# Optimization experiments

Measured on AMD Instinct MI355X. Metric: run time of the kernel, lower is better.

## Reference

```python
import jax, jax.numpy as jnp
import numpy as np

N, F_IN, F_OUT = 8192, 256, 256
ALPHA = 0.2  # LeakyReLU negative slope
NEG = -9e15

def setup_inputs() -> dict:
    key = jax.random.key(0)
    k1, k2, k3, k4, k5 = jax.random.split(key, 5)
    h = jax.random.normal(k1, (N, F_IN), dtype=jnp.float32)
    adj = jax.random.randint(k2, (N, N), 0, 2, dtype=jnp.int32)
    W_w = jax.random.normal(k3, (F_IN, F_OUT), dtype=jnp.float32) / np.sqrt(F_IN)
    W_b = jax.random.normal(k4, (F_OUT,), dtype=jnp.float32) * 0.01
    a = jax.random.normal(k5, (2 * F_OUT, 1), dtype=jnp.float32) / np.sqrt(2 * F_OUT)
    return {"h": h, "adj": adj, "W_w": W_w, "W_b": W_b, "a": a}

def reference(h, adj, W_w, W_b, a):
    # Wh: [N, F_OUT]
    Wh = h @ W_w + W_b
    a1 = a[:F_OUT, 0]   # scores for source node i (row)
    a2 = a[F_OUT:, 0]   # scores for target node j (col)
    # e[i,j] = leakyrelu(Wh_i . a1 + Wh_j . a2)  -- separable form of the
    # original repeat/cat construction, identical math without the NxNx2F tensor.
    e = jax.nn.leaky_relu((Wh @ a1)[:, None] + (Wh @ a2)[None, :], negative_slope=ALPHA)
    attention = jnp.where(adj > 0, e, NEG)
    attention = jax.nn.softmax(attention, axis=1)
    # dropout is identity in eval / p=0
    h_prime = attention @ Wh  # [N, F_OUT]
    return h_prime
```

## Files before the change

### kernel.cpp

```cpp
#include <hip/hip_runtime.h>
#include <stdint.h>

#define NN 8192
#define FD 256
#define LOG2E 1.44269504088896340736f
#define PPAD 136

typedef __attribute__((ext_vector_type(8))) __bf16 bf16x8;
typedef __attribute__((ext_vector_type(4))) float f32x4;

__device__ __forceinline__ unsigned short f2bf(float x) {
    unsigned u = __float_as_uint(x);
    u = u + 0x7fffu + ((u >> 16) & 1u);
    return (unsigned short)(u >> 16);
}
__device__ __forceinline__ bf16x8 ld_bf8(const unsigned short* p) {
    uint4 v = *(const uint4*)p;
    return __builtin_bit_cast(bf16x8, v);
}
__device__ __forceinline__ unsigned pack2(float a, float b) {
    return (unsigned)f2bf(a) | ((unsigned)f2bf(b) << 16);
}

__global__ __launch_bounds__(256) void wtrans_kernel(const float* __restrict__ W,
                                                     unsigned short* __restrict__ WbT) {
    int idx = blockIdx.x * 256 + threadIdx.x;
    int k = idx >> 8, f = idx & 255;
    WbT[f * 256 + k] = f2bf(W[idx]);
}

__global__ __launch_bounds__(256) void gemm1_kernel(const float* __restrict__ h,
                                                    const unsigned short* __restrict__ WbT,
                                                    const float* __restrict__ bias,
                                                    unsigned short* __restrict__ WhT) {
    __shared__ float Wh_s[256 * 33];
    int t = threadIdx.x;
    int l = t & 63, w = t >> 6;
    int i0 = blockIdx.x * 32;
    int fbase = w * 64;
    int cl = l & 15, q = l >> 4;

    f32x4 acc[2][4] = {};
    const float* hA0 = h + (size_t)(i0 + cl) * FD;
    const float* hA1 = h + (size_t)(i0 + 16 + cl) * FD;

    #pragma unroll
    for (int ks = 0; ks < 8; ++ks) {
        int kk = ks * 32 + q * 8;
        union { unsigned short u[8]; bf16x8 v; } ua0, ua1;
        float4 x0 = *(const float4*)(hA0 + kk);
        float4 x1 = *(const float4*)(hA0 + kk + 4);
        float4 y0 = *(const float4*)(hA1 + kk);
        float4 y1 = *(const float4*)(hA1 + kk + 4);
        ua0.u[0]=f2bf(x0.x); ua0.u[1]=f2bf(x0.y); ua0.u[2]=f2bf(x0.z); ua0.u[3]=f2bf(x0.w);
        ua0.u[4]=f2bf(x1.x); ua0.u[5]=f2bf(x1.y); ua0.u[6]=f2bf(x1.z); ua0.u[7]=f2bf(x1.w);
        ua1.u[0]=f2bf(y0.x); ua1.u[1]=f2bf(y0.y); ua1.u[2]=f2bf(y0.z); ua1.u[3]=f2bf(y0.w);
        ua1.u[4]=f2bf(y1.x); ua1.u[5]=f2bf(y1.y); ua1.u[6]=f2bf(y1.z); ua1.u[7]=f2bf(y1.w);
        #pragma unroll
        for (int bg = 0; bg < 4; ++bg) {
            bf16x8 bF = ld_bf8(WbT + (fbase + bg * 16 + cl) * 256 + kk);
            acc[0][bg] = __builtin_amdgcn_mfma_f32_16x16x32_bf16(ua0.v, bF, acc[0][bg], 0, 0, 0);
            acc[1][bg] = __builtin_amdgcn_mfma_f32_16x16x32_bf16(ua1.v, bF, acc[1][bg], 0, 0, 0);
        }
    }

    #pragma unroll
    for (int mt = 0; mt < 2; ++mt)
        #pragma unroll
        for (int bg = 0; bg < 4; ++bg)
            #pragma unroll
            for (int e = 0; e < 4; ++e) {
                int il = mt * 16 + q * 4 + e;
                int fl = fbase + bg * 16 + cl;
                Wh_s[fl * 33 + il] = acc[mt][bg][e] + bias[fl];
            }
    __syncthreads();
    {
        const float* src = &Wh_s[t * 33];
        unsigned short* dst = WhT + (size_t)t * NN + i0;
        #pragma unroll
        for (int ig = 0; ig < 4; ++ig) {
            union { unsigned short u[8]; uint4 v; } p;
            #pragma unroll
            for (int e = 0; e < 8; ++e) p.u[e] = f2bf(src[ig * 8 + e]);
            *(uint4*)(dst + ig * 8) = p.v;
        }
    }
}

__global__ __launch_bounds__(256) void f1f2_kernel(const unsigned short* __restrict__ WhT,
                                                   const float* __restrict__ a,
                                                   float* __restrict__ f1p,
                                                   float* __restrict__ f2p) {
    int i = blockIdx.x * 256 + threadIdx.x;
    float s1 = 0.f, s2 = 0.f;
    #pragma unroll 8
    for (int f = 0; f < 256; ++f) {
        float wv = __uint_as_float((unsigned)WhT[(size_t)f * NN + i] << 16);
        s1 += wv * a[f];
        s2 += wv * a[256 + f];
    }
    f1p[i] = s1 * LOG2E;
    f2p[i] = s2 * LOG2E;
}

__global__ __launch_bounds__(512, 2) void gat_kernel(const int* __restrict__ adj,
                                                     const unsigned short* __restrict__ WhT,
                                                     const float* __restrict__ f1p,
                                                     const float* __restrict__ f2p,
                                                     float* __restrict__ out) {
    __shared__ float rowsum_s[32];
    __shared__ unsigned short P_s[32 * PPAD];
    __shared__ float red_s[32 * 256];

    int t = threadIdx.x;
    int l = t & 63, w = t >> 6;
    int i0 = blockIdx.x * 32;
    if (t < 32) rowsum_s[t] = 0.f;

    int pr = t >> 5;
    int pc = (t & 31) * 4;
    float f1v0 = f1p[i0 + pr];
    float f1v1 = f1p[i0 + 16 + pr];

    int ns = w & 3, kh = w >> 2;
    int fbase = ns * 64;
    int cl = l & 15, q = l >> 4;
    f32x4 acc[2][4] = {};
    const unsigned short* wrow = WhT + (size_t)(fbase + cl) * NN;

    const int* aprow = adj + (size_t)(i0 + pr) * NN + pc;
    int4 adjv0 = *(const int4*)(aprow);
    int4 adjv1 = *(const int4*)(aprow + (size_t)16 * NN);
    float4 f2v = *(const float4*)(f2p + pc);

    for (int jt = 0; jt < NN / 128; ++jt) {
        int j0 = jt * 128;
        int4 a0 = adjv0, a1 = adjv1;
        float4 fv = f2v;
        if (jt < NN / 128 - 1) {
            adjv0 = *(const int4*)(aprow + j0 + 128);
            adjv1 = *(const int4*)(aprow + (size_t)16 * NN + j0 + 128);
            f2v = *(const float4*)(f2p + j0 + 128 + pc);
        }
        float ws0[4], ws1[4], rs0 = 0.f, rs1 = 0.f;
        {
            float fe[4] = {fv.x, fv.y, fv.z, fv.w};
            int ae0[4] = {a0.x, a0.y, a0.z, a0.w};
            int ae1[4] = {a1.x, a1.y, a1.z, a1.w};
            #pragma unroll
            for (int e = 0; e < 4; ++e) {
                float s0 = f1v0 + fe[e]; s0 = fmaxf(s0, 0.2f * s0);
                float w0 = exp2f(s0); w0 = ae0[e] > 0 ? w0 : 0.f;
                ws0[e] = w0; rs0 += w0;
                float s1 = f1v1 + fe[e]; s1 = fmaxf(s1, 0.2f * s1);
                float w1 = exp2f(s1); w1 = ae1[e] > 0 ? w1 : 0.f;
                ws1[e] = w1; rs1 += w1;
            }
        }
        #pragma unroll
        for (int m = 1; m <= 16; m <<= 1) { rs0 += __shfl_xor(rs0, m); rs1 += __shfl_xor(rs1, m); }

        __syncthreads();
        *(uint2*)(P_s + pr * PPAD + pc) = make_uint2(pack2(ws0[0], ws0[1]), pack2(ws0[2], ws0[3]));
        *(uint2*)(P_s + (16 + pr) * PPAD + pc) = make_uint2(pack2(ws1[0], ws1[1]), pack2(ws1[2], ws1[3]));
        if ((l & 31) == 0) { atomicAdd(&rowsum_s[pr], rs0); atomicAdd(&rowsum_s[16 + pr], rs1); }
        __syncthreads();

        #pragma unroll
        for (int ksi = 0; ksi < 2; ++ksi) {
            int kk = kh * 64 + ksi * 32 + q * 8;
            bf16x8 af0 = ld_bf8(P_s + cl * PPAD + kk);
            bf16x8 af1 = ld_bf8(P_s + (16 + cl) * PPAD + kk);
            #pragma unroll
            for (int bg = 0; bg < 4; ++bg) {
                bf16x8 bF = ld_bf8(wrow + (size_t)bg * 16 * NN + j0 + kk);
                acc[0][bg] = __builtin_amdgcn_mfma_f32_16x16x32_bf16(af0, bF, acc[0][bg], 0, 0, 0);
                acc[1][bg] = __builtin_amdgcn_mfma_f32_16x16x32_bf16(af1, bF, acc[1][bg], 0, 0, 0);
            }
        }
    }

    __syncthreads();
    if (kh == 1) {
        #pragma unroll
        for (int mt = 0; mt < 2; ++mt)
            #pragma unroll
            for (int bg = 0; bg < 4; ++bg)
                #pragma unroll
                for (int e = 0; e < 4; ++e)
                    red_s[(mt * 16 + q * 4 + e) * 256 + fbase + bg * 16 + cl] = acc[mt][bg][e];
    }
    __syncthreads();
    if (kh == 0) {
        #pragma unroll
        for (int mt = 0; mt < 2; ++mt)
            #pragma unroll
            for (int e = 0; e < 4; ++e) {
                int row = mt * 16 + q * 4 + e;
                float inv = 1.0f / rowsum_s[row];
                #pragma unroll
                for (int bg = 0; bg < 4; ++bg) {
                    float v = acc[mt][bg][e] + red_s[row * 256 + fbase + bg * 16 + cl];
                    out[(size_t)(i0 + row) * FD + fbase + bg * 16 + cl] = v * inv;
                }
            }
    }
}

extern "C" void kernel_launch(void* const* d_in, const int* in_sizes, int n_in,
                              void* d_out, int out_size, void* d_ws, size_t ws_size,
                              hipStream_t stream) {
    const float* h   = (const float*)d_in[0];
    const int*   adj = (const int*)d_in[1];
    const float* W   = (const float*)d_in[2];
    const float* b   = (const float*)d_in[3];
    const float* a   = (const float*)d_in[4];
    float* out = (float*)d_out;

    char* ws = (char*)d_ws;
    unsigned short* WhT = (unsigned short*)ws;
    unsigned short* WbT = (unsigned short*)(ws + 4 * 1024 * 1024);
    float* f1p = (float*)(ws + 4 * 1024 * 1024 + 128 * 1024);
    float* f2p = f1p + NN;

    wtrans_kernel<<<256, 256, 0, stream>>>(W, WbT);
    gemm1_kernel<<<256, 256, 0, stream>>>(h, WbT, b, WhT);
    f1f2_kernel<<<32, 256, 0, stream>>>(WhT, a, f1p, f2p);
    gat_kernel<<<256, 512, 0, stream>>>(adj, WhT, f1p, f2p, out);
}
```

Measured before the change: 497.0 us.

## Fuse f1/f2 into GEMM epilogue and compute attention weights in MFMA registers

The f1/f2 score dot-products move into the gemm1 epilogue, reading the fp32 tile from shared memory, which removes one kernel launch and a strided re-read of WhT. The GAT kernel is restructured so each wave computes its own attention weights directly in MFMA A-operand layout for 16 rows. This drops the shared P tile, the barriers, the LDS atomics and the split-K reduction. Adjacency and f2 loads are prefetched four steps ahead and B fragments one step ahead. In exchange, each of the four waves recomputes the same exp values for its feature slice, and each block now covers 16 rows with 512 blocks.

```diff
diff --git a/kernel.cpp b/kernel.cpp
--- a/kernel.cpp
+++ b/kernel.cpp
@@ -4,7 +4,6 @@
 #define NN 8192
 #define FD 256
 #define LOG2E 1.44269504088896340736f
-#define PPAD 136
 
 typedef __attribute__((ext_vector_type(8))) __bf16 bf16x8;
 typedef __attribute__((ext_vector_type(4))) float f32x4;
@@ -17,9 +16,6 @@
 __device__ __forceinline__ bf16x8 ld_bf8(const unsigned short* p) {
     uint4 v = *(const uint4*)p;
     return __builtin_bit_cast(bf16x8, v);
-}
-__device__ __forceinline__ unsigned pack2(float a, float b) {
-    return (unsigned)f2bf(a) | ((unsigned)f2bf(b) << 16);
 }
 
 __global__ __launch_bounds__(256) void wtrans_kernel(const float* __restrict__ W,
@@ -32,8 +28,12 @@
 __global__ __launch_bounds__(256) void gemm1_kernel(const float* __restrict__ h,
                                                     const unsigned short* __restrict__ WbT,
                                                     const float* __restrict__ bias,
-                                                    unsigned short* __restrict__ WhT) {
+                                                    const float* __restrict__ av,
+                                                    unsigned short* __restrict__ WhT,
+                                                    float* __restrict__ f1p,
+                                                    float* __restrict__ f2p) {
     __shared__ float Wh_s[256 * 33];
+    __shared__ float red_s[2 * 8 * 32];
     int t = threadIdx.x;
     int l = t & 63, w = t >> 6;
     int i0 = blockIdx.x * 32;
@@ -86,125 +86,112 @@
             *(uint4*)(dst + ig * 8) = p.v;
         }
     }
-}
-
-__global__ __launch_bounds__(256) void f1f2_kernel(const unsigned short* __restrict__ WhT,
-                                                   const float* __restrict__ a,
-                                                   float* __restrict__ f1p,
-                                                   float* __restrict__ f2p) {
-    int i = blockIdx.x * 256 + threadIdx.x;
-    float s1 = 0.f, s2 = 0.f;
-    #pragma unroll 8
-    for (int f = 0; f < 256; ++f) {
-        float wv = __uint_as_float((unsigned)WhT[(size_t)f * NN + i] << 16);
-        s1 += wv * a[f];
-        s2 += wv * a[256 + f];
-    }
-    f1p[i] = s1 * LOG2E;
-    f2p[i] = s2 * LOG2E;
-}
-
-__global__ __launch_bounds__(512, 2) void gat_kernel(const int* __restrict__ adj,
+    {
+        int i = t & 31, fc = t >> 5;
+        float s1 = 0.f, s2 = 0.f;
+        #pragma unroll
+        for (int fo = 0; fo < 32; ++fo) {
+            int f = fc * 32 + fo;
+            float wv = Wh_s[f * 33 + i];
+            s1 += wv * av[f];
+            s2 += wv * av[256 + f];
+        }
+        red_s[fc * 32 + i] = s1;
+        red_s[256 + fc * 32 + i] = s2;
+    }
+    __syncthreads();
+    if (t < 32) {
+        float s = 0.f;
+        #pragma unroll
+        for (int fc = 0; fc < 8; ++fc) s += red_s[fc * 32 + t];
+        f1p[i0 + t] = s * LOG2E;
+    } else if (t < 64) {
+        int i = t - 32;
+        float s = 0.f;
+        #pragma unroll
+        for (int fc = 0; fc < 8; ++fc) s += red_s[256 + fc * 32 + i];
+        f2p[i0 + i] = s * LOG2E;
+    }
+}
+
+__global__ __launch_bounds__(256, 2) void gat_kernel(const int* __restrict__ adj,
                                                      const unsigned short* __restrict__ WhT,
                                                      const float* __restrict__ f1p,
                                                      const float* __restrict__ f2p,
                                                      float* __restrict__ out) {
-    __shared__ float rowsum_s[32];
-    __shared__ unsigned short P_s[32 * PPAD];
-    __shared__ float red_s[32 * 256];
-
     int t = threadIdx.x;
     int l = t & 63, w = t >> 6;
-    int i0 = blockIdx.x * 32;
-    if (t < 32) rowsum_s[t] = 0.f;
-
-    int pr = t >> 5;
-    int pc = (t & 31) * 4;
-    float f1v0 = f1p[i0 + pr];
-    float f1v1 = f1p[i0 + 16 + pr];
-
-    int ns = w & 3, kh = w >> 2;
-    int fbase = ns * 64;
+    int i0 = blockIdx.x * 16;
     int cl = l & 15, q = l >> 4;
-    f32x4 acc[2][4] = {};
-    const unsigned short* wrow = WhT + (size_t)(fbase + cl) * NN;
-
-    const int* aprow = adj + (size_t)(i0 + pr) * NN + pc;
-    int4 adjv0 = *(const int4*)(aprow);
-    int4 adjv1 = *(const int4*)(aprow + (size_t)16 * NN);
-    float4 f2v = *(const float4*)(f2p + pc);
-
-    for (int jt = 0; jt < NN / 128; ++jt) {
-        int j0 = jt * 128;
-        int4 a0 = adjv0, a1 = adjv1;
-        float4 fv = f2v;
-        if (jt < NN / 128 - 1) {
-            adjv0 = *(const int4*)(aprow + j0 + 128);
-            adjv1 = *(const int4*)(aprow + (size_t)16 * NN + j0 + 128);
-            f2v = *(const float4*)(f2p + j0 + 128 + pc);
-        }
-        float ws0[4], ws1[4], rs0 = 0.f, rs1 = 0.f;
-        {
-            float fe[4] = {fv.x, fv.y, fv.z, fv.w};
-            int ae0[4] = {a0.x, a0.y, a0.z, a0.w};
-            int ae1[4] = {a1.x, a1.y, a1.z, a1.w};
-            #pragma unroll
-            for (int e = 0; e < 4; ++e) {
-                float s0 = f1v0 + fe[e]; s0 = fmaxf(s0, 0.2f * s0);
-                float w0 = exp2f(s0); w0 = ae0[e] > 0 ? w0 : 0.f;
-                ws0[e] = w0; rs0 += w0;
-                float s1 = f1v1 + fe[e]; s1 = fmaxf(s1, 0.2f * s1);
-                float w1 = exp2f(s1); w1 = ae1[e] > 0 ? w1 : 0.f;
-                ws1[e] = w1; rs1 += w1;
-            }
-        }
-        #pragma unroll
-        for (int m = 1; m <= 16; m <<= 1) { rs0 += __shfl_xor(rs0, m); rs1 += __shfl_xor(rs1, m); }
-
-        __syncthreads();
-        *(uint2*)(P_s + pr * PPAD + pc) = make_uint2(pack2(ws0[0], ws0[1]), pack2(ws0[2], ws0[3]));
-        *(uint2*)(P_s + (16 + pr) * PPAD + pc) = make_uint2(pack2(ws1[0], ws1[1]), pack2(ws1[2], ws1[3]));
-        if ((l & 31) == 0) { atomicAdd(&rowsum_s[pr], rs0); atomicAdd(&rowsum_s[16 + pr], rs1); }
-        __syncthreads();
-
-        #pragma unroll
-        for (int ksi = 0; ksi < 2; ++ksi) {
-            int kk = kh * 64 + ksi * 32 + q * 8;
-            bf16x8 af0 = ld_bf8(P_s + cl * PPAD + kk);
-            bf16x8 af1 = ld_bf8(P_s + (16 + cl) * PPAD + kk);
-            #pragma unroll
-            for (int bg = 0; bg < 4; ++bg) {
-                bf16x8 bF = ld_bf8(wrow + (size_t)bg * 16 * NN + j0 + kk);
-                acc[0][bg] = __builtin_amdgcn_mfma_f32_16x16x32_bf16(af0, bF, acc[0][bg], 0, 0, 0);
-                acc[1][bg] = __builtin_amdgcn_mfma_f32_16x16x32_bf16(af1, bF, acc[1][bg], 0, 0, 0);
-            }
-        }
-    }
-
-    __syncthreads();
-    if (kh == 1) {
-        #pragma unroll
-        for (int mt = 0; mt < 2; ++mt)
-            #pragma unroll
-            for (int bg = 0; bg < 4; ++bg)
-                #pragma unroll
-                for (int e = 0; e < 4; ++e)
-                    red_s[(mt * 16 + q * 4 + e) * 256 + fbase + bg * 16 + cl] = acc[mt][bg][e];
-    }
-    __syncthreads();
-    if (kh == 0) {
-        #pragma unroll
-        for (int mt = 0; mt < 2; ++mt)
-            #pragma unroll
-            for (int e = 0; e < 4; ++e) {
-                int row = mt * 16 + q * 4 + e;
-                float inv = 1.0f / rowsum_s[row];
-                #pragma unroll
-                for (int bg = 0; bg < 4; ++bg) {
-                    float v = acc[mt][bg][e] + red_s[row * 256 + fbase + bg * 16 + cl];
-                    out[(size_t)(i0 + row) * FD + fbase + bg * 16 + cl] = v * inv;
-                }
-            }
+    int fbase = w * 64;
+
+    float f1v = f1p[i0 + cl];
+    const int* arow = adj + (size_t)(i0 + cl) * NN + q * 8;
+    const float* f2row = f2p + q * 8;
+    const unsigned short* wrow = WhT + (size_t)(fbase + cl) * NN + q * 8;
+
+    f32x4 acc[4] = {};
+    float rs = 0.f;
+
+    int4   aq[4][2];
+    float4 fq[4][2];
+    #pragma unroll
+    for (int p = 0; p < 4; ++p) {
+        aq[p][0] = *(const int4*)(arow + p * 32);
+        aq[p][1] = *(const int4*)(arow + p * 32 + 4);
+        fq[p][0] = *(const float4*)(f2row + p * 32);
+        fq[p][1] = *(const float4*)(f2row + p * 32 + 4);
+    }
+    bf16x8 bcur[4];
+    #pragma unroll
+    for (int bg = 0; bg < 4; ++bg) bcur[bg] = ld_bf8(wrow + (size_t)bg * 16 * NN);
+
+    #pragma unroll 4
+    for (int jt = 0; jt < NN / 32; ++jt) {
+        int slot = jt & 3;
+        int4 a0 = aq[slot][0], a1 = aq[slot][1];
+        float4 F0 = fq[slot][0], F1 = fq[slot][1];
+
+        int pj = jt + 4 < NN / 32 ? jt + 4 : jt;
+        aq[slot][0] = *(const int4*)(arow + pj * 32);
+        aq[slot][1] = *(const int4*)(arow + pj * 32 + 4);
+        fq[slot][0] = *(const float4*)(f2row + pj * 32);
+        fq[slot][1] = *(const float4*)(f2row + pj * 32 + 4);
+
+        int bj = jt + 1 < NN / 32 ? jt + 1 : jt;
+        bf16x8 bnext[4];
+        #pragma unroll
+        for (int bg = 0; bg < 4; ++bg)
+            bnext[bg] = ld_bf8(wrow + (size_t)bg * 16 * NN + bj * 32);
+
+        float fa[8] = {F0.x, F0.y, F0.z, F0.w, F1.x, F1.y, F1.z, F1.w};
+        int   ad[8] = {a0.x, a0.y, a0.z, a0.w, a1.x, a1.y, a1.z, a1.w};
+        union { unsigned short u[8]; bf16x8 v; } af;
+        #pragma unroll
+        for (int e = 0; e < 8; ++e) {
+            float s = f1v + fa[e];
+            s = fmaxf(s, 0.2f * s);
+            float wv = exp2f(s);
+            wv = ad[e] > 0 ? wv : 0.f;
+            rs += wv;
+            af.u[e] = f2bf(wv);
+        }
+        #pragma unroll
+        for (int bg = 0; bg < 4; ++bg)
+            acc[bg] = __builtin_amdgcn_mfma_f32_16x16x32_bf16(af.v, bcur[bg], acc[bg], 0, 0, 0);
+        #pragma unroll
+        for (int bg = 0; bg < 4; ++bg) bcur[bg] = bnext[bg];
+    }
+
+    rs += __shfl_xor(rs, 16);
+    rs += __shfl_xor(rs, 32);
+    #pragma unroll
+    for (int e = 0; e < 4; ++e) {
+        int r = q * 4 + e;
+        float inv = 1.0f / __shfl(rs, r);
+        #pragma unroll
+        for (int bg = 0; bg < 4; ++bg)
+            out[(size_t)(i0 + r) * FD + fbase + bg * 16 + cl] = acc[bg][e] * inv;
     }
 }
 
@@ -225,7 +212,6 @@
     float* f2p = f1p + NN;
 
     wtrans_kernel<<<256, 256, 0, stream>>>(W, WbT);
-    gemm1_kernel<<<256, 256, 0, stream>>>(h, WbT, b, WhT);
-    f1f2_kernel<<<32, 256, 0, stream>>>(WhT, a, f1p, f2p);
-    gat_kernel<<<256, 512, 0, stream>>>(adj, WhT, f1p, f2p, out);
-}
+    gemm1_kernel<<<256, 256, 0, stream>>>(h, WbT, b, a, WhT, f1p, f2p);
+    gat_kernel<<<512, 256, 0, stream>>>(adj, WhT, f1p, f2p, out);
+}
```

Measured after the change: 752.5 us. 51.4% more time.
